# Kernel tuning notes

Measured on AMD Instinct MI355X. Metric: run time of the kernel, lower is better.

## Reference

```python
import jax, jax.numpy as jnp
import numpy as np

N_P, N_A = 100000, 20000
F_P, D_A, H = 512, 128, 256
E_W, E_C = 200000, 400000


def setup_inputs() -> dict:
    key = jax.random.key(0)
    ks = jax.random.split(key, 32)
    s = 0.05  # param init scale
    inp = {
        # node inputs
        'paper_feat': (jax.random.uniform(ks[0], (N_P, F_P)) < 0.02).astype(jnp.float32),  # sparse multi-hot
        'author_emb': jax.random.normal(ks[1], (N_A, D_A), jnp.float32),
        # edges: author --writes--> paper, paper --cites--> paper
        'writes_src': jax.random.randint(ks[2], (E_W,), 0, N_A, jnp.int32),
        'writes_dst': jax.random.randint(ks[3], (E_W,), 0, N_P, jnp.int32),
        'writes_w': jax.random.uniform(ks[4], (E_W,), jnp.float32),
        'cites_src': jax.random.randint(ks[5], (E_C,), 0, N_P, jnp.int32),
        'cites_dst': jax.random.randint(ks[6], (E_C,), 0, N_P, jnp.int32),
        'cites_w': jax.random.uniform(ks[7], (E_C,), jnp.float32),
        # layer 1 params (in dims per node type: paper=F_P, author=D_A)
        'W1_self_p': jax.random.normal(ks[8], (F_P, H), jnp.float32) * s,
        'b1_self_p': jnp.zeros((H,), jnp.float32),
        'W1_self_a': jax.random.normal(ks[9], (D_A, H), jnp.float32) * s,
        'b1_self_a': jnp.zeros((H,), jnp.float32),
        'W1_rel_writes': jax.random.normal(ks[10], (D_A, H), jnp.float32) * s,
        'b1_rel_writes': jnp.zeros((H,), jnp.float32),
        'W1_rel_cites': jax.random.normal(ks[11], (F_P, H), jnp.float32) * s,
        'b1_rel_cites': jnp.zeros((H,), jnp.float32),
        # layer 2 params (all in dims = H)
        'W2_self_p': jax.random.normal(ks[12], (H, H), jnp.float32) * s,
        'b2_self_p': jnp.zeros((H,), jnp.float32),
        'W2_self_a': jax.random.normal(ks[13], (H, H), jnp.float32) * s,
        'b2_self_a': jnp.zeros((H,), jnp.float32),
        'W2_rel_writes': jax.random.normal(ks[14], (H, H), jnp.float32) * s,
        'b2_rel_writes': jnp.zeros((H,), jnp.float32),
        'W2_rel_cites': jax.random.normal(ks[15], (H, H), jnp.float32) * s,
        'b2_rel_cites': jnp.zeros((H,), jnp.float32),
    }
    return inp


def _hetero_layer(xp, xa, edges, Wsp, bsp, Wsa, bsa, Wrw, brw, Wrc, brc, activation):
    """One HeteroLayer: per-type self linear + per-relation gather/scale/scatter-add."""
    writes_src, writes_dst, writes_w, cites_src, cites_dst, cites_w = edges
    out_p = xp @ Wsp + bsp          # [N_P, H]
    out_a = xa @ Wsa + bsa          # [N_A, H]
    # relation author --writes--> paper
    msg_w = xa @ Wrw + brw          # dense per-relation linear on source nodes
    gathered_w = msg_w[writes_src] * writes_w[:, None]          # gather + edge weight
    out_p = out_p + jax.ops.segment_sum(gathered_w, writes_dst, num_segments=out_p.shape[0])
    # relation paper --cites--> paper
    msg_c = xp @ Wrc + brc
    gathered_c = msg_c[cites_src] * cites_w[:, None]
    out_p = out_p + jax.ops.segment_sum(gathered_c, cites_dst, num_segments=out_p.shape[0])
    if activation:
        out_p = jax.nn.elu(out_p)
        out_a = jax.nn.elu(out_a)
    return out_p, out_a


def reference(paper_feat, author_emb,
              writes_src, writes_dst, writes_w,
              cites_src, cites_dst, cites_w,
              W1_self_p, b1_self_p, W1_self_a, b1_self_a,
              W1_rel_writes, b1_rel_writes, W1_rel_cites, b1_rel_cites,
              W2_self_p, b2_self_p, W2_self_a, b2_self_a,
              W2_rel_writes, b2_rel_writes, W2_rel_cites, b2_rel_cites):
    edges = (writes_src, writes_dst, writes_w, cites_src, cites_dst, cites_w)
    xp, xa = _hetero_layer(paper_feat, author_emb, edges,
                           W1_self_p, b1_self_p, W1_self_a, b1_self_a,
                           W1_rel_writes, b1_rel_writes, W1_rel_cites, b1_rel_cites,
                           activation=True)
    xp, xa = _hetero_layer(xp, xa, edges,
                           W2_self_p, b2_self_p, W2_self_a, b2_self_a,
                           W2_rel_writes, b2_rel_writes, W2_rel_cites, b2_rel_cites,
                           activation=False)
    return xp, xa
```

## Files before the change

kernel.cpp:

```cpp
#include <hip/hip_runtime.h>
#include <cstdint>
#include <cstddef>

constexpr int Hd  = 256;
constexpr int N_P = 100000;
constexpr int N_A = 20000;
constexpr int F_P = 512;
constexpr int D_A = 128;

typedef short bf16x8 __attribute__((ext_vector_type(8)));
typedef float f32x4  __attribute__((ext_vector_type(4)));

__device__ __forceinline__ unsigned short f2b(float x) {
    unsigned u = __float_as_uint(x);
    u += 0x7fffu + ((u >> 16) & 1u);
    return (unsigned short)(u >> 16);
}
__device__ __forceinline__ float b2f(unsigned short h) {
    return __uint_as_float((unsigned)h << 16);
}
__device__ __forceinline__ unsigned pk2(float lo, float hi) {
    return (__float_as_uint(lo) >> 16) | (__float_as_uint(hi) & 0xffff0000u);
}
__device__ __forceinline__ void bsplit(float x, unsigned short& hi, unsigned short& lo) {
    const unsigned u = __float_as_uint(x);
    hi = (unsigned short)(u >> 16);
    const float r = x - __uint_as_float(u & 0xffff0000u);
    lo = (unsigned short)(__float_as_uint(r) >> 16);
}

__device__ __forceinline__ void gld16(const void* g, void* l) {
    __builtin_amdgcn_global_load_lds(
        (const __attribute__((address_space(1))) unsigned int*)g,
        (__attribute__((address_space(3))) unsigned int*)l, 16, 0, 0);
}

__global__ void prep_kernel(const float* __restrict__ W1sa, const float* __restrict__ W1rw,
                            const float* __restrict__ W2sa, const float* __restrict__ W2rw,
                            const float* __restrict__ W2rc, const float* __restrict__ W2sp,
                            const float* __restrict__ W1sp, const float* __restrict__ W1rc,
                            const float* __restrict__ b1sa, const float* __restrict__ b1rw,
                            const float* __restrict__ b2sa, const float* __restrict__ b2rw,
                            const float* __restrict__ b2rc, const float* __restrict__ b2sp,
                            const float* __restrict__ b1sp, const float* __restrict__ b1rc,
                            unsigned short* __restrict__ w1h,  unsigned short* __restrict__ w1l,
                            unsigned short* __restrict__ wA2h, unsigned short* __restrict__ wA2l,
                            unsigned short* __restrict__ wP2h,
                            unsigned short* __restrict__ wP1h,
                            float* __restrict__ bc1, float* __restrict__ bcA2,
                            float* __restrict__ bcP2, float* __restrict__ bcP1) {
    const int b = blockIdx.x;
    const int l = threadIdx.x;
    if (b < 384) {
        const float *Wa, *Wb; unsigned short *wh, *wl; int rel;
        if (b < 128) { Wa = W1sa; Wb = W1rw; wh = w1h;  wl = w1l;  rel = b; }
        else         { Wa = W2sa; Wb = W2rw; wh = wA2h; wl = wA2l; rel = b - 128; }
        const int ks  = rel >> 5;
        const int nfg = rel & 31;
        const float* W = (nfg < 16) ? Wa : Wb;
        const int col  = (nfg & 15) * 16 + (l & 15);
        const size_t base = ((size_t)rel * 64 + l) * 8;
        #pragma unroll
        for (int j = 0; j < 8; ++j) {
            const int k = ks * 32 + ((l >> 4) * 8) + j;
            unsigned short h, lw;
            bsplit(W[(size_t)k * Hd + col], h, lw);
            wh[base + j] = h;
            wl[base + j] = lw;
        }
    } else if (b < 640) {
        const int rel = b - 384;
        const int ks  = rel >> 5;
        const int nfg = rel & 31;
        const float* W = (nfg < 16) ? W2rc : W2sp;
        const int col  = (nfg & 15) * 16 + (l & 15);
        const size_t base = ((size_t)rel * 64 + l) * 8;
        #pragma unroll
        for (int j = 0; j < 8; ++j) {
            const int k = ks * 32 + ((l >> 4) * 8) + j;
            wP2h[base + j] = f2b(W[(size_t)k * Hd + col]);
        }
    } else if (b < 1152) {
        const int rel = b - 640;
        const int ks  = rel >> 5;
        const int nfg = rel & 31;
        const float* W = (nfg < 16) ? W1sp : W1rc;
        const int col  = (nfg & 15) * 16 + (l & 15);
        const size_t base = ((size_t)rel * 64 + l) * 8;
        #pragma unroll
        for (int j = 0; j < 8; ++j) {
            const int k = ks * 32 + ((l >> 4) * 8) + j;
            wP1h[base + j] = f2b(W[(size_t)k * Hd + col]);
        }
    } else {
        const int t     = (b - 1152) * 64 + l;
        const int which = t >> 9;
        const int idx   = t & 511;
        const float* src; float* dst;
        if (which == 0)      { src = (idx < 256) ? b1sa : b1rw; dst = bc1;  }
        else if (which == 1) { src = (idx < 256) ? b2sa : b2rw; dst = bcA2; }
        else if (which == 2) { src = (idx < 256) ? b2rc : b2sp; dst = bcP2; }
        else                 { src = (idx < 256) ? b1sp : b1rc; dst = bcP1; }
        dst[idx] = src[idx & 255];
    }
}

__global__ void conv_kernel(const float* __restrict__ in, unsigned short* __restrict__ out,
                            const long n4) {
    const long stride = (long)gridDim.x * blockDim.x;
    for (long i = (long)blockIdx.x * blockDim.x + threadIdx.x; i < n4; i += stride) {
        const float4 v = ((const float4*)in)[i];
        ((ushort4*)out)[i] = make_ushort4(
            (unsigned short)(__float_as_uint(v.x) >> 16),
            (unsigned short)(__float_as_uint(v.y) >> 16),
            (unsigned short)(__float_as_uint(v.z) >> 16),
            (unsigned short)(__float_as_uint(v.w) >> 16));
    }
}

template<int AMODE>
__global__ void __launch_bounds__(256, 3)
mfma_tile2_kernel(const void* __restrict__ Av, const int KA, const int nks,
                  const unsigned short* __restrict__ wtab,
                  const float* __restrict__ bcat,
                  void* __restrict__ Oa, void* __restrict__ Ob,
                  const int bfA, const int bfB, const int Mtot, const int gM) {
    const int d = blockIdx.x;
    const int r = ((d >> 5) << 3) + (d & 7);
    if (r >= gM) return;
    const int c = (d >> 3) & 3;

    extern __shared__ char smem[];
    const int tid = threadIdx.x;
    const int wid = tid >> 6;
    const int l   = tid & 63;
    const long m0 = (long)r * 128;
    const int wr  = wid >> 1, wc = wid & 1;

    const unsigned short* bg0 = wtab + ((size_t)(c * 8 + 2 * wid) * 512) + l * 8;
    const unsigned short* bg1 = bg0 + 512;

    const unsigned short* ag0 = nullptr; const unsigned short* ag1 = nullptr;
    const float* Af = nullptr;
    long grow0 = 0, grow1 = 0; int kg = 0;
    if constexpr (AMODE == 1) {
        const unsigned short* A = (const unsigned short*)Av;
        long r0 = m0 + (2 * wid) * 16 + (l & 15);     if (r0 > Mtot - 1) r0 = Mtot - 1;
        long r1 = m0 + (2 * wid + 1) * 16 + (l & 15); if (r1 > Mtot - 1) r1 = Mtot - 1;
        ag0 = A + r0 * KA + ((l >> 4) * 8);
        ag1 = A + r1 * KA + ((l >> 4) * 8);
    } else {
        Af = (const float*)Av;
        const int f0 = tid >> 6;
        grow0 = m0 + f0 * 16 + (l & 15);       if (grow0 > Mtot - 1) grow0 = Mtot - 1;
        grow1 = m0 + (f0 + 4) * 16 + (l & 15); if (grow1 > Mtot - 1) grow1 = Mtot - 1;
        kg = (l >> 4) * 8;
    }

    float4 a00, a01, a10, a11;

#define STAGE_B(BUF, KS) { \
    char* Bb_ = smem + (BUF) * 16384 + 8192; \
    gld16(bg0 + (size_t)(KS) * 16384, Bb_ + wid * 2048); \
    gld16(bg1 + (size_t)(KS) * 16384, Bb_ + wid * 2048 + 1024); }
#define STAGE_A1(BUF, KS) { \
    char* Ab_ = smem + (BUF) * 16384; \
    gld16(ag0 + (KS) * 32, Ab_ + wid * 2048); \
    gld16(ag1 + (KS) * 32, Ab_ + wid * 2048 + 1024); }
#define LOAD_A0(KS) { \
    const float* p0_ = Af + grow0 * KA + (KS) * 32 + kg; \
    const float* p1_ = Af + grow1 * KA + (KS) * 32 + kg; \
    a00 = *(const float4*)p0_; a01 = *(const float4*)(p0_ + 4); \
    a10 = *(const float4*)p1_; a11 = *(const float4*)(p1_ + 4); }
#define WRITE_A0(BUF) { \
    char* Ab_ = smem + (BUF) * 16384; \
    *(uint4*)(Ab_ + tid * 16) = make_uint4(pk2(a00.x, a00.y), pk2(a00.z, a00.w), \
                                           pk2(a01.x, a01.y), pk2(a01.z, a01.w)); \
    *(uint4*)(Ab_ + (tid + 256) * 16) = make_uint4(pk2(a10.x, a10.y), pk2(a10.z, a10.w), \
                                                   pk2(a11.x, a11.y), pk2(a11.z, a11.w)); }

    f32x4 acc[4][4];
    #pragma unroll
    for (int nf = 0; nf < 4; ++nf) {
        const float b = bcat[c * 128 + wc * 64 + nf * 16 + (l & 15)];
        #pragma unroll
        for (int mf = 0; mf < 4; ++mf) acc[mf][nf] = (f32x4){b, b, b, b};
    }

    STAGE_B(0, 0)
    if constexpr (AMODE == 1) { STAGE_A1(0, 0) }
    else { LOAD_A0(0) WRITE_A0(0) }
    __syncthreads();

    int cur = 0;
    for (int ks = 0; ks < nks; ++ks) {
        const bool more = (ks + 1 < nks);
        if (more) {
            STAGE_B(cur ^ 1, ks + 1)
            if constexpr (AMODE == 1) { STAGE_A1(cur ^ 1, ks + 1) }
            else { LOAD_A0(ks + 1) }
        }
        {
            const char* Ab = smem + cur * 16384;
            const char* Bb = Ab + 8192;
            bf16x8 af[4], bfv[4];
            #pragma unroll
            for (int mf = 0; mf < 4; ++mf)
                af[mf] = *(const bf16x8*)(Ab + ((wr * 4 + mf) * 64 + l) * 16);
            #pragma unroll
            for (int nf = 0; nf < 4; ++nf)
                bfv[nf] = *(const bf16x8*)(Bb + ((wc * 4 + nf) * 64 + l) * 16);
            #pragma unroll
            for (int nf = 0; nf < 4; ++nf) {
                #pragma unroll
                for (int mf = 0; mf < 4; ++mf)
                    acc[mf][nf] = __builtin_amdgcn_mfma_f32_16x16x32_bf16(af[mf], bfv[nf], acc[mf][nf], 0, 0, 0);
            }
        }
        if (more) { if constexpr (AMODE == 0) WRITE_A0(cur ^ 1) }
        __syncthreads();
        cur ^= 1;
    }
#undef STAGE_B
#undef STAGE_A1
#undef LOAD_A0
#undef WRITE_A0

    #pragma unroll
    for (int mf = 0; mf < 4; ++mf) {
        #pragma unroll
        for (int nf = 0; nf < 4; ++nf) {
            const int gcol = c * 128 + wc * 64 + nf * 16 + (l & 15);
            void* O; int col, isbf;
            if (gcol < 256) { O = Oa; col = gcol;       isbf = bfA; }
            else            { O = Ob; col = gcol - 256; isbf = bfB; }
            const long row = m0 + wr * 64 + mf * 16 + ((l >> 4) * 4);
            const f32x4 v = acc[mf][nf];
            #pragma unroll
            for (int rr = 0; rr < 4; ++rr) {
                if (row + rr < Mtot) {
                    const float x = v[rr];
                    if (isbf) ((unsigned short*)O)[(row + rr) * Hd + col] = f2b(x);
                    else      ((float*)O)[(row + rr) * Hd + col] = x;
                }
            }
        }
    }
}

__global__ void mfma_dual_kernel(const void* __restrict__ Av, const int K,
                                 const unsigned short* __restrict__ whi,
                                 const unsigned short* __restrict__ wlo,
                                 const float* __restrict__ bcat,
                                 void* __restrict__ Oa, void* __restrict__ Ob,
                                 const int actA, const int actB,
                                 const int bfA, const int bfB) {
    extern __shared__ char smem[];
    char* sh = smem;
    char* sl = smem + 32 * K * 2;
    const int  tid = threadIdx.x;
    const int  wid = tid >> 6;
    const int  l   = tid & 63;
    const long m0  = (long)blockIdx.x * 32;
    const int  rowStride = 2 * K;

    const int kq4 = K >> 2;
    const float* A = (const float*)Av;
    for (int i = tid; i < 32 * kq4; i += 256) {
        const int row = i / kq4;
        const int kq  = i - row * kq4;
        const float4 v = *(const float4*)(A + (m0 + row) * K + kq * 4);
        unsigned short h0, h1, h2, h3, l0, l1, l2, l3;
        bsplit(v.x, h0, l0); bsplit(v.y, h1, l1);
        bsplit(v.z, h2, l2); bsplit(v.w, h3, l3);
        const int ofs = row * rowStride + ((kq * 8) ^ ((row & 7) << 4));
        *(ushort4*)(sh + ofs) = make_ushort4(h0, h1, h2, h3);
        *(ushort4*)(sl + ofs) = make_ushort4(l0, l1, l2, l3);
    }
    __syncthreads();

    f32x4 acc[2][8];
    #pragma unroll
    for (int nf = 0; nf < 8; ++nf) {
        const float b = bcat[wid * 128 + nf * 16 + (l & 15)];
        acc[0][nf] = (f32x4){b, b, b, b};
        acc[1][nf] = (f32x4){b, b, b, b};
    }

    const int kb  = (l >> 4) * 16;
    const int r0  = l & 15;
    const int r1  = 16 + r0;
    const int sw  = (l & 7) << 4;
    const int ro0 = r0 * rowStride;
    const int ro1 = r1 * rowStride;
    for (int ks = 0; ks < (K >> 5); ++ks) {
        const int bk = (ks * 64 + kb) ^ sw;
        const bf16x8 ah0 = *(const bf16x8*)(sh + ro0 + bk);
        const bf16x8 ah1 = *(const bf16x8*)(sh + ro1 + bk);
        const bf16x8 al0 = *(const bf16x8*)(sl + ro0 + bk);
        const bf16x8 al1 = *(const bf16x8*)(sl + ro1 + bk);
        const size_t wbase = (((size_t)ks * 32 + wid * 8) * 64 + l) * 8;
        #pragma unroll
        for (int nf = 0; nf < 8; ++nf) {
            const bf16x8 bh = *(const bf16x8*)(whi + wbase + (size_t)nf * 512);
            const bf16x8 bl = *(const bf16x8*)(wlo + wbase + (size_t)nf * 512);
            acc[0][nf] = __builtin_amdgcn_mfma_f32_16x16x32_bf16(ah0, bh, acc[0][nf], 0, 0, 0);
            acc[1][nf] = __builtin_amdgcn_mfma_f32_16x16x32_bf16(ah1, bh, acc[1][nf], 0, 0, 0);
            acc[0][nf] = __builtin_amdgcn_mfma_f32_16x16x32_bf16(al0, bh, acc[0][nf], 0, 0, 0);
            acc[1][nf] = __builtin_amdgcn_mfma_f32_16x16x32_bf16(al1, bh, acc[1][nf], 0, 0, 0);
            acc[0][nf] = __builtin_amdgcn_mfma_f32_16x16x32_bf16(ah0, bl, acc[0][nf], 0, 0, 0);
            acc[1][nf] = __builtin_amdgcn_mfma_f32_16x16x32_bf16(ah1, bl, acc[1][nf], 0, 0, 0);
        }
    }

    #pragma unroll
    for (int mf = 0; mf < 2; ++mf) {
        #pragma unroll
        for (int nf = 0; nf < 8; ++nf) {
            const int colg = wid * 128 + nf * 16 + (l & 15);
            void* O;
            int col, act, isbf;
            if (colg < 256) { O = Oa; col = colg;       act = actA; isbf = bfA; }
            else            { O = Ob; col = colg - 256; act = actB; isbf = bfB; }
            const long row = m0 + mf * 16 + ((l >> 4) * 4);
            const f32x4 v = acc[mf][nf];
            #pragma unroll
            for (int r = 0; r < 4; ++r) {
                float x = v[r];
                if (act) x = x > 0.f ? x : expm1f(x);
                if (isbf) ((unsigned short*)O)[(row + r) * Hd + col] = f2b(x);
                else      ((float*)O)[(row + r) * Hd + col] = x;
            }
        }
    }
}

__global__ void hist_kernel(const int* __restrict__ wdst, const int EW,
                            const int* __restrict__ cdst, const int EC,
                            int* __restrict__ cnt) {
    for (int i = blockIdx.x * blockDim.x + threadIdx.x; i < EW + EC; i += gridDim.x * blockDim.x) {
        const int d = (i < EW) ? wdst[i] : cdst[i - EW];
        atomicAdd(&cnt[d], 1);
    }
}

__global__ void scan1_kernel(int* __restrict__ data, const int n, int* __restrict__ bsum) {
    __shared__ int s[256];
    const int t = threadIdx.x;
    const int base = blockIdx.x * 1024 + t * 4;
    int v0 = (base + 0 < n) ? data[base + 0] : 0;
    int v1 = (base + 1 < n) ? data[base + 1] : 0;
    int v2 = (base + 2 < n) ? data[base + 2] : 0;
    int v3 = (base + 3 < n) ? data[base + 3] : 0;
    const int tsum = v0 + v1 + v2 + v3;
    s[t] = tsum;
    __syncthreads();
    for (int off = 1; off < 256; off <<= 1) {
        int y = (t >= off) ? s[t - off] : 0;
        __syncthreads();
        if (t >= off) s[t] += y;
        __syncthreads();
    }
    const int e = s[t] - tsum;
    if (base + 0 < n) data[base + 0] = e;
    if (base + 1 < n) data[base + 1] = e + v0;
    if (base + 2 < n) data[base + 2] = e + v0 + v1;
    if (base + 3 < n) data[base + 3] = e + v0 + v1 + v2;
    if (t == 255) bsum[blockIdx.x] = s[255];
}

__global__ void scan2_kernel(int* __restrict__ bsum, const int nb) {
    __shared__ int s[256];
    const int t = threadIdx.x;
    const int v = (t < nb) ? bsum[t] : 0;
    s[t] = v;
    __syncthreads();
    for (int off = 1; off < 256; off <<= 1) {
        int y = (t >= off) ? s[t - off] : 0;
        __syncthreads();
        if (t >= off) s[t] += y;
        __syncthreads();
    }
    if (t < nb) bsum[t] = s[t] - v;
}

__global__ void scan3_kernel(int* __restrict__ data, const int n, const int* __restrict__ bsum) {
    const int i = blockIdx.x * blockDim.x + threadIdx.x;
    if (i < n) data[i] += bsum[i >> 10];
}

__global__ void fill_kernel(const int* __restrict__ wsrc, const int* __restrict__ wdst,
                            const float* __restrict__ ww, const int EW,
                            const int* __restrict__ csrc, const int* __restrict__ cdst,
                            const float* __restrict__ cw, const int EC,
                            int* __restrict__ cur, int2* __restrict__ edges) {
    for (int i = blockIdx.x * blockDim.x + threadIdx.x; i < EW + EC; i += gridDim.x * blockDim.x) {
        int d, sp; float w;
        if (i < EW) { d = wdst[i]; sp = wsrc[i]; w = ww[i]; }
        else        { const int j = i - EW; d = cdst[j]; sp = N_A + csrc[j]; w = cw[j]; }
        const int p = atomicAdd(&cur[d], 1);
        edges[p] = make_int2(sp, __float_as_int(w));
    }
}

struct AgChunk { ushort4 g0, g1, g2, g3; float w0, w1, w2, w3; };

__device__ __forceinline__ void ag_issue(const int2* __restrict__ eq, const int base, const int n,
                                         const unsigned short* __restrict__ msg,
                                         const int lane, AgChunk& C) {
#define AG_ONE(J, GG, WW) { \
    const int idx = base + (J); \
    const int2 ee = eq[min(idx, n - 1)]; \
    WW = (idx < n) ? __int_as_float(ee.y) : 0.f; \
    GG = ((const ushort4*)(msg + (size_t)ee.x * Hd))[lane]; }
    AG_ONE(0, C.g0, C.w0)
    AG_ONE(1, C.g1, C.w1)
    AG_ONE(2, C.g2, C.w2)
    AG_ONE(3, C.g3, C.w3)
#undef AG_ONE
}

__device__ __forceinline__ void ag_acc(const AgChunk& C, float4& acc) {
#define AG_A(GG, WW) { \
    acc.x = fmaf(WW, b2f(GG.x), acc.x); acc.y = fmaf(WW, b2f(GG.y), acc.y); \
    acc.z = fmaf(WW, b2f(GG.z), acc.z); acc.w = fmaf(WW, b2f(GG.w), acc.w); }
    AG_A(C.g0, C.w0) AG_A(C.g1, C.w1) AG_A(C.g2, C.w2) AG_A(C.g3, C.w3)
#undef AG_A
}

template<int MODE>
__global__ void aggregate_kernel(void* __restrict__ iov, void* __restrict__ outv,
                                 const unsigned short* __restrict__ msgAll,
                                 const int* __restrict__ off,
                                 const int2* __restrict__ edges,
                                 const int do_elu) {
    __shared__ int2 eq[1024];
    const int wid  = threadIdx.x >> 6;
    const int lane = threadIdx.x & 63;
    const int p0   = blockIdx.x * 4;
    const int sAll = (p0 == 0) ? 0 : off[p0 - 1];
    const int tot  = off[p0 + 3] - sAll;
    const bool fits = (tot <= 1024);
    if (fits)
        for (int i = threadIdx.x; i < tot; i += 256) eq[i] = edges[sAll + i];
    __syncthreads();

    const int p = p0 + wid;
    const int s = (p == 0) ? 0 : off[p - 1];
    const int e = off[p];
    const int n = e - s;

    float4 acc;
    if constexpr (MODE >= 1) {
        const ushort4 t = ((const ushort4*)((const unsigned short*)iov + (size_t)p * Hd))[lane];
        acc = make_float4(b2f(t.x), b2f(t.y), b2f(t.z), b2f(t.w));
    } else {
        acc = ((const float4*)((const float*)iov + (size_t)p * Hd))[lane];
    }

    if (n > 0) {
        if (fits) {
            const int2* eqw = eq + (s - sAll);
            int nc = (n + 3) >> 2;
            nc += (nc & 1);
            AgChunk CA, CB;
            ag_issue(eqw, 0, n, msgAll, lane, CA);
            int c = 1;
            for (; c + 1 < nc; c += 2) {
                ag_issue(eqw, 4 * c, n, msgAll, lane, CB);
                ag_acc(CA, acc);
                ag_issue(eqw, 4 * (c + 1), n, msgAll, lane, CA);
                ag_acc(CB, acc);
            }
            ag_issue(eqw, 4 * (nc - 1), n, msgAll, lane, CB);
            ag_acc(CA, acc);
            ag_acc(CB, acc);
        } else {
            for (int i = s; i < e; ++i) {
                const int2 ee = edges[i];
                const ushort4 g = ((const ushort4*)(msgAll + (size_t)ee.x * Hd))[lane];
                const float w = __int_as_float(ee.y);
                acc.x = fmaf(w, b2f(g.x), acc.x); acc.y = fmaf(w, b2f(g.y), acc.y);
                acc.z = fmaf(w, b2f(g.z), acc.z); acc.w = fmaf(w, b2f(g.w), acc.w);
            }
        }
    }
    if (do_elu) {
        acc.x = acc.x > 0.f ? acc.x : expm1f(acc.x);
        acc.y = acc.y > 0.f ? acc.y : expm1f(acc.y);
        acc.z = acc.z > 0.f ? acc.z : expm1f(acc.z);
        acc.w = acc.w > 0.f ? acc.w : expm1f(acc.w);
    }
    if constexpr (MODE == 1) {
        ((ushort4*)((unsigned short*)iov + (size_t)p * Hd))[lane] =
            make_ushort4(f2b(acc.x), f2b(acc.y), f2b(acc.z), f2b(acc.w));
    } else if constexpr (MODE == 2) {
        ((float4*)((float*)outv + (size_t)p * Hd))[lane] = acc;
    } else {
        ((float4*)((float*)iov + (size_t)p * Hd))[lane] = acc;
    }
}

extern "C" void kernel_launch(void* const* d_in, const int* in_sizes, int n_in,
                              void* d_out, int out_size, void* d_ws, size_t ws_size,
                              hipStream_t stream) {
    const float* pf    = (const float*)d_in[0];
    const float* ae    = (const float*)d_in[1];
    const int*   wsrc  = (const int*)d_in[2];
    const int*   wdst  = (const int*)d_in[3];
    const float* ww    = (const float*)d_in[4];
    const int*   csrc  = (const int*)d_in[5];
    const int*   cdst  = (const int*)d_in[6];
    const float* cw    = (const float*)d_in[7];
    const float* W1sp  = (const float*)d_in[8];
    const float* b1sp  = (const float*)d_in[9];
    const float* W1sa  = (const float*)d_in[10];
    const float* b1sa  = (const float*)d_in[11];
    const float* W1rw  = (const float*)d_in[12];
    const float* b1rw  = (const float*)d_in[13];
    const float* W1rc  = (const float*)d_in[14];
    const float* b1rc  = (const float*)d_in[15];
    const float* W2sp  = (const float*)d_in[16];
    const float* b2sp  = (const float*)d_in[17];
    const float* W2sa  = (const float*)d_in[18];
    const float* b2sa  = (const float*)d_in[19];
    const float* W2rw  = (const float*)d_in[20];
    const float* b2rw  = (const float*)d_in[21];
    const float* W2rc  = (const float*)d_in[22];
    const float* b2rc  = (const float*)d_in[23];

    const int E_W = in_sizes[2];
    const int E_C = in_sizes[5];

    float* outP = (float*)d_out;
    float* outA = outP + (size_t)N_P * Hd;

    float*          xa1    = (float*)d_ws;
    unsigned short* xp1b   = (unsigned short*)(xa1 + (size_t)N_A * Hd);
    unsigned short* msgAll = xp1b + (size_t)N_P * Hd;
    unsigned short* msgP   = msgAll + (size_t)N_A * Hd;
    int*            off    = (int*)(msgAll + (size_t)(N_A + N_P) * Hd);
    int2*           edges  = (int2*)(off + N_P);
    int*            bsum   = (int*)(edges + (E_W + E_C));
    float*          bc1    = (float*)(bsum + 256);
    float*          bcA2   = bc1 + 512;
    float*          bcP2   = bcA2 + 512;
    float*          bcP1   = bcP2 + 512;
    unsigned short* w1h    = (unsigned short*)(bcP1 + 512);
    unsigned short* w1l    = w1h  + (size_t)128 * 512;
    unsigned short* wA2h   = w1l  + (size_t)128 * 512;
    unsigned short* wA2l   = wA2h + (size_t)256 * 512;
    unsigned short* wP2h   = wA2l + (size_t)256 * 512;
    unsigned short* wP1h   = wP2h + (size_t)256 * 512;
    unsigned short* pfb    = (unsigned short*)
        (((uintptr_t)(wP1h + (size_t)512 * 512) + 63) & ~(uintptr_t)63);
    unsigned short* selfP  = pfb + (size_t)N_P * F_P;
    const size_t needPfb  = ((char*)(pfb  + (size_t)N_P * F_P)) - (char*)d_ws;
    const size_t needSelf = ((char*)(selfP + (size_t)N_P * Hd)) - (char*)d_ws;
    const bool usePfb  = (ws_size >= needPfb);
    const bool useSelf = (ws_size >= needSelf);

    const dim3 blk(256);
    const int  nb   = (N_P + 1023) / 1024;
    const int  gM   = (N_P + 127) / 128;
    const int  gPad = ((gM + 7) / 8) * 8 * 4;

    prep_kernel<<<1184, 64, 0, stream>>>(W1sa, W1rw, W2sa, W2rw, W2rc, W2sp, W1sp, W1rc,
                                         b1sa, b1rw, b2sa, b2rw, b2rc, b2sp, b1sp, b1rc,
                                         w1h, w1l, wA2h, wA2l, wP2h, wP1h,
                                         bc1, bcA2, bcP2, bcP1);

    hipMemsetAsync(off, 0, (size_t)N_P * sizeof(int), stream);
    hist_kernel<<<1024, blk, 0, stream>>>(wdst, E_W, cdst, E_C, off);
    scan1_kernel<<<nb, blk, 0, stream>>>(off, N_P, bsum);
    scan2_kernel<<<1,  blk, 0, stream>>>(bsum, nb);
    scan3_kernel<<<(N_P + 255) / 256, blk, 0, stream>>>(off, N_P, bsum);
    fill_kernel<<<1024, blk, 0, stream>>>(wsrc, wdst, ww, E_W, csrc, cdst, cw, E_C,
                                          off, edges);

    if (usePfb) {
        conv_kernel<<<2048, blk, 0, stream>>>(pf, pfb, (long)N_P * F_P / 4);
        mfma_tile2_kernel<1><<<gPad, blk, 32768, stream>>>(pfb, 512, 16, wP1h, bcP1,
                                                           xp1b, msgP, 1, 1, N_P, gM);
    } else {
        mfma_tile2_kernel<0><<<gPad, blk, 32768, stream>>>(pf, 512, 16, wP1h, bcP1,
                                                           xp1b, msgP, 1, 1, N_P, gM);
    }
    mfma_dual_kernel<<<N_A / 32, blk, 32 * 128 * 4, stream>>>(ae, 128, w1h, w1l, bc1,
                                                              xa1, msgAll, 1, 0, 0, 1);
    aggregate_kernel<1><<<N_P / 4, blk, 0, stream>>>(xp1b, nullptr, msgAll, off, edges, 1);

    mfma_dual_kernel<<<N_A / 32, blk, 32 * 256 * 4, stream>>>(xa1, 256, wA2h, wA2l, bcA2,
                                                              outA, msgAll, 0, 0, 0, 1);
    if (useSelf) {
        mfma_tile2_kernel<1><<<gPad, blk, 32768, stream>>>(xp1b, 256, 8, wP2h, bcP2,
                                                           msgP, selfP, 1, 1, N_P, gM);
        aggregate_kernel<2><<<N_P / 4, blk, 0, stream>>>(selfP, outP, msgAll, off, edges, 0);
    } else {
        mfma_tile2_kernel<1><<<gPad, blk, 32768, stream>>>(xp1b, 256, 8, wP2h, bcP2,
                                                           msgP, outP, 1, 0, N_P, gM);
        aggregate_kernel<0><<<N_P / 4, blk, 0, stream>>>(outP, nullptr, msgAll, off, edges, 0);
    }
}
```

Baseline: 453.8 us.

## Fuse feature bf16 conversion with edge histogram; triple-buffer aggregate gathers

The fp32-to-bf16 conversion of paper features is merged into one launch with the destination-degree histogram, with block ranges split between the two jobs, so they run concurrently and one launch is removed. The aggregate kernel's gather loop moves from double to triple buffering of edge chunks to keep more loads in flight. The extra buffer raises register pressure, and padding chunk counts to multiples of three may issue more empty chunks.

Result: slower. 462.9 us (+2.0%).

```diff
diff --git a/kernel.cpp b/kernel.cpp
--- a/kernel.cpp
+++ b/kernel.cpp
@@ -105,16 +105,37 @@
     }
 }
 
-__global__ void conv_kernel(const float* __restrict__ in, unsigned short* __restrict__ out,
-                            const long n4) {
-    const long stride = (long)gridDim.x * blockDim.x;
-    for (long i = (long)blockIdx.x * blockDim.x + threadIdx.x; i < n4; i += stride) {
-        const float4 v = ((const float4*)in)[i];
-        ((ushort4*)out)[i] = make_ushort4(
-            (unsigned short)(__float_as_uint(v.x) >> 16),
-            (unsigned short)(__float_as_uint(v.y) >> 16),
-            (unsigned short)(__float_as_uint(v.z) >> 16),
-            (unsigned short)(__float_as_uint(v.w) >> 16));
+__global__ void convhist_kernel(const float* __restrict__ in, unsigned short* __restrict__ out,
+                                const long n4,
+                                const int* __restrict__ wdst, const int EW,
+                                const int* __restrict__ cdst, const int EC,
+                                int* __restrict__ cnt) {
+    const int b = blockIdx.x;
+    if (b < 1024) {
+        const long stride = (long)1024 * blockDim.x;
+        for (long i = (long)b * blockDim.x + threadIdx.x; i < n4; i += stride) {
+            const float4 v = ((const float4*)in)[i];
+            ((ushort4*)out)[i] = make_ushort4(
+                (unsigned short)(__float_as_uint(v.x) >> 16),
+                (unsigned short)(__float_as_uint(v.y) >> 16),
+                (unsigned short)(__float_as_uint(v.z) >> 16),
+                (unsigned short)(__float_as_uint(v.w) >> 16));
+        }
+    } else {
+        const int stride = 1024 * blockDim.x;
+        for (int i = (b - 1024) * blockDim.x + threadIdx.x; i < EW + EC; i += stride) {
+            const int d = (i < EW) ? wdst[i] : cdst[i - EW];
+            atomicAdd(&cnt[d], 1);
+        }
+    }
+}
+
+__global__ void hist_kernel(const int* __restrict__ wdst, const int EW,
+                            const int* __restrict__ cdst, const int EC,
+                            int* __restrict__ cnt) {
+    for (int i = blockIdx.x * blockDim.x + threadIdx.x; i < EW + EC; i += gridDim.x * blockDim.x) {
+        const int d = (i < EW) ? wdst[i] : cdst[i - EW];
+        atomicAdd(&cnt[d], 1);
     }
 }
 
@@ -335,15 +356,6 @@
     }
 }
 
-__global__ void hist_kernel(const int* __restrict__ wdst, const int EW,
-                            const int* __restrict__ cdst, const int EC,
-                            int* __restrict__ cnt) {
-    for (int i = blockIdx.x * blockDim.x + threadIdx.x; i < EW + EC; i += gridDim.x * blockDim.x) {
-        const int d = (i < EW) ? wdst[i] : cdst[i - EW];
-        atomicAdd(&cnt[d], 1);
-    }
-}
-
 __global__ void scan1_kernel(int* __restrict__ data, const int n, int* __restrict__ bsum) {
     __shared__ int s[256];
     const int t = threadIdx.x;
@@ -462,19 +474,22 @@
         if (fits) {
             const int2* eqw = eq + (s - sAll);
             int nc = (n + 3) >> 2;
-            nc += (nc & 1);
-            AgChunk CA, CB;
+            nc = ((nc + 2) / 3) * 3;
+            AgChunk CA, CB, CC;
             ag_issue(eqw, 0, n, msgAll, lane, CA);
-            int c = 1;
-            for (; c + 1 < nc; c += 2) {
-                ag_issue(eqw, 4 * c, n, msgAll, lane, CB);
+            ag_issue(eqw, 4, n, msgAll, lane, CB);
+            ag_issue(eqw, 8, n, msgAll, lane, CC);
+            for (int c = 0; c + 3 < nc; c += 3) {
                 ag_acc(CA, acc);
-                ag_issue(eqw, 4 * (c + 1), n, msgAll, lane, CA);
+                ag_issue(eqw, 4 * (c + 3), n, msgAll, lane, CA);
                 ag_acc(CB, acc);
+                ag_issue(eqw, 4 * (c + 4), n, msgAll, lane, CB);
+                ag_acc(CC, acc);
+                ag_issue(eqw, 4 * (c + 5), n, msgAll, lane, CC);
             }
-            ag_issue(eqw, 4 * (nc - 1), n, msgAll, lane, CB);
             ag_acc(CA, acc);
             ag_acc(CB, acc);
+            ag_acc(CC, acc);
         } else {
             for (int i = s; i < e; ++i) {
                 const int2 ee = edges[i];
@@ -571,7 +586,12 @@
                                          bc1, bcA2, bcP2, bcP1);
 
     hipMemsetAsync(off, 0, (size_t)N_P * sizeof(int), stream);
-    hist_kernel<<<1024, blk, 0, stream>>>(wdst, E_W, cdst, E_C, off);
+    if (usePfb) {
+        convhist_kernel<<<2048, blk, 0, stream>>>(pf, pfb, (long)N_P * F_P / 4,
+                                                  wdst, E_W, cdst, E_C, off);
+    } else {
+        hist_kernel<<<1024, blk, 0, stream>>>(wdst, E_W, cdst, E_C, off);
+    }
     scan1_kernel<<<nb, blk, 0, stream>>>(off, N_P, bsum);
     scan2_kernel<<<1,  blk, 0, stream>>>(bsum, nb);
     scan3_kernel<<<(N_P + 255) / 256, blk, 0, stream>>>(off, N_P, bsum);
@@ -579,7 +599,6 @@
                                           off, edges);
 
     if (usePfb) {
-        conv_kernel<<<2048, blk, 0, stream>>>(pf, pfb, (long)N_P * F_P / 4);
         mfma_tile2_kernel<1><<<gPad, blk, 32768, stream>>>(pfb, 512, 16, wP1h, bcP1,
                                                            xp1b, msgP, 1, 1, N_P, gM);
     } else {
```
